# Optimization experiments

Hardware: AMD Instinct MI355X
Metric: run time of the kernel (lower is better)

## Reference

```python
import jax, jax.numpy as jnp
import numpy as np

D_MODEL = 1024
N_HEAD = 16
D_K = D_MODEL // N_HEAD
D_FF = 2048
EPS = 1e-6
SCALE = np.sqrt(D_K).astype(np.float32)


def layer_norm(x, alpha, beta):
    # Faithful to source: unbiased std (ddof=1), eps added to std
    mean = jnp.mean(x, axis=-1, keepdims=True)
    std = jnp.std(x, axis=-1, keepdims=True, ddof=1) + EPS
    return alpha * (x - mean) / std + beta


def setup_inputs() -> dict:
    key = jax.random.key(0)
    ks = jax.random.split(key, 12)
    s = 0.02
    return {
        "x": jax.random.normal(ks[0], (4, 1024, D_MODEL), dtype=jnp.float32),
        "Wq": jax.random.normal(ks[1], (D_MODEL, D_MODEL), dtype=jnp.float32) * s,
        "bq": jax.random.normal(ks[2], (D_MODEL,), dtype=jnp.float32) * s,
        "Wo": jax.random.normal(ks[3], (D_MODEL, D_MODEL), dtype=jnp.float32) * s,
        "bo": jax.random.normal(ks[4], (D_MODEL,), dtype=jnp.float32) * s,
        "W1": jax.random.normal(ks[5], (D_MODEL, D_FF), dtype=jnp.float32) * s,
        "b1": jax.random.normal(ks[6], (D_FF,), dtype=jnp.float32) * s,
        "W2": jax.random.normal(ks[7], (D_FF, D_MODEL), dtype=jnp.float32) * s,
        "b2": jax.random.normal(ks[8], (D_MODEL,), dtype=jnp.float32) * s,
        "alpha": jnp.ones((D_MODEL,), dtype=jnp.float32),
        "beta": jnp.ones((D_MODEL,), dtype=jnp.float32),
    }


def reference(x, Wq, bq, Wo, bo, W1, b1, W2, b2, alpha, beta):
    b, s, d = x.shape
    # Source bug kept: q, k, v all use q_linear
    def proj(t):
        return (t @ Wq + bq).reshape(b, s, N_HEAD, D_K).transpose(0, 2, 1, 3)
    q = proj(x)  # [b,h,s,dk]
    k = proj(x)
    v = proj(x)
    scores = jnp.einsum('bhqd,bhkd->bhqk', q, k) / SCALE
    scores = jax.nn.softmax(scores, axis=-1)
    z = jnp.einsum('bhqk,bhkd->bhqd', scores, v)
    concat = z.transpose(0, 2, 1, 3).reshape(b, s, d)
    attn_out = concat @ Wo + bo
    x = layer_norm(x + attn_out, alpha, beta)
    ff = jax.nn.relu(x @ W1 + b1) @ W2 + b2
    x = layer_norm(x + ff, alpha, beta)  # source reuses norm_1
    return x
```

## Files before the change

### kernel.cpp

```cpp
#include <hip/hip_runtime.h>
#include <hip/hip_bf16.h>
#include <stdint.h>

#define TOK   4096
#define DMODEL 1024
#define DFF    2048
#define NHEAD  16
#define DK     64

typedef unsigned short u16;
typedef __attribute__((ext_vector_type(8))) short short8;
typedef __attribute__((ext_vector_type(4))) float f32x4;

typedef __attribute__((address_space(1))) void gvoid;
typedef __attribute__((address_space(3))) void lvoid;

#define QSCALE   0.35355339f
#define QUNSCALE 2.82842712f

__device__ __forceinline__ u16 f2b(float f) {
    uint32_t x = __builtin_bit_cast(uint32_t, f);
    x += 0x7FFFu + ((x >> 16) & 1u);
    return (u16)(x >> 16);
}
__device__ __forceinline__ float b2f(u16 u) {
    uint32_t x = ((uint32_t)u) << 16;
    return __builtin_bit_cast(float, x);
}
__device__ __forceinline__ uint32_t f2b2(float lo, float hi) {
    return (uint32_t)f2b(lo) | ((uint32_t)f2b(hi) << 16);
}

__device__ __forceinline__ void gload16(const void* g, void* l) {
    __builtin_amdgcn_global_load_lds((gvoid*)g, (lvoid*)l, 16, 0, 0);
}

__device__ __forceinline__ void cvt_tr_dev(
    const float* __restrict__ W, u16* __restrict__ Wt, int K, int N,
    int bx, int by, int tid, u16 T[64][68])
{
    const int tx = tid & 15, ty = tid >> 4;
    const int n0 = bx * 64, k0 = by * 64;
#pragma unroll
    for (int i = 0; i < 4; i++) {
        int k = ty + i * 16;
        float4 v = *(const float4*)&W[(size_t)(k0 + k) * N + n0 + tx * 4];
        T[tx * 4 + 0][k] = f2b(v.x);
        T[tx * 4 + 1][k] = f2b(v.y);
        T[tx * 4 + 2][k] = f2b(v.z);
        T[tx * 4 + 3][k] = f2b(v.w);
    }
    __syncthreads();
#pragma unroll
    for (int i = 0; i < 4; i++) {
        int n = ty + i * 16;
        ushort4 o;
        o.x = T[n][tx * 4 + 0]; o.y = T[n][tx * 4 + 1];
        o.z = T[n][tx * 4 + 2]; o.w = T[n][tx * 4 + 3];
        *(ushort4*)&Wt[(size_t)(n0 + n) * K + k0 + tx * 4] = o;
    }
}

__global__ __launch_bounds__(256) void prep_all(
    const float* __restrict__ Wq, const float* __restrict__ Wo,
    const float* __restrict__ W1, const float* __restrict__ W2,
    u16* __restrict__ Wqt, u16* __restrict__ Wot,
    u16* __restrict__ W1t, u16* __restrict__ W2t,
    const float* __restrict__ x, u16* __restrict__ xb)
{
    __shared__ u16 T[64][68];
    const int id = blockIdx.x, tid = threadIdx.x;
    if (id < 256) {
        cvt_tr_dev(Wq, Wqt, 1024, 1024, id & 15, id >> 4, tid, T);
    } else if (id < 512) {
        int t = id - 256;
        cvt_tr_dev(Wo, Wot, 1024, 1024, t & 15, t >> 4, tid, T);
    } else if (id < 1024) {
        int t = id - 512;
        cvt_tr_dev(W1, W1t, 1024, 2048, t & 31, t >> 5, tid, T);
    } else if (id < 1536) {
        int t = id - 1024;
        cvt_tr_dev(W2, W2t, 2048, 1024, t & 15, t >> 4, tid, T);
    } else {
        size_t base = (size_t)(id - 1536) * 1024 + tid;
#pragma unroll
        for (int j = 0; j < 4; j++) {
            float4 v = ((const float4*)x)[base + j * 256];
            ((uint2*)xb)[base + j * 256] =
                make_uint2(f2b2(v.x, v.y), f2b2(v.z, v.w));
        }
    }
}

template<int BM, int BN, bool RELU, bool OUTBF16, bool QOUT>
__global__ __launch_bounds__(256) void gemm_mfma(
    const u16* __restrict__ A, const u16* __restrict__ Bt,
    const float* __restrict__ bias, void* __restrict__ Cv,
    u16* __restrict__ CT, float oscale,
    int M, int N, int K)
{
    constexpr int MF = BM / 32;
    constexpr int NF = BN / 32;
    constexpr int ASTR = BM * 64;
    constexpr int BSTR = BN * 64;
    __shared__ __align__(16) u16 As[2 * ASTR];
    __shared__ __align__(16) u16 Bs[2 * BSTR];

    const int tid  = threadIdx.x;
    const int lane = tid & 63;
    const int wid  = tid >> 6;
    const int wm = wid >> 1, wn = wid & 1;
    const int frow = lane & 15, fk = lane >> 4;

    const int gx = N / BN;
    const int gy = M / BM;
    const int rpx = gy >> 3;
    const int L = blockIdx.x;
    const int xcd = L & 7, within = L >> 3;
    const int yy = xcd * rpx + within / gx;
    const int xx = within % gx;

    const int row0 = yy * BM;
    const int col0 = xx * BN;

    const u16* gA[MF]; u16* lA[MF];
    const u16* gB[NF]; u16* lB[NF];
#pragma unroll
    for (int inst = 0; inst < MF; inst++) {
        int s = inst * 256 + tid;
        int r = s >> 3;
        int kc = ((s & 7) ^ (r & 7)) * 8;
        gA[inst] = A + (size_t)(row0 + r) * K + kc;
        lA[inst] = As + inst * 2048 + wid * 512;
    }
#pragma unroll
    for (int inst = 0; inst < NF; inst++) {
        int s = inst * 256 + tid;
        int r = s >> 3;
        int kc = ((s & 7) ^ (r & 7)) * 8;
        gB[inst] = Bt + (size_t)(col0 + r) * K + kc;
        lB[inst] = Bs + inst * 2048 + wid * 512;
    }

    int aoff[MF][2], boff[NF][2];
#pragma unroll
    for (int m = 0; m < MF; m++) {
        int r = wm * (BM / 2) + m * 16 + frow;
#pragma unroll
        for (int kk = 0; kk < 2; kk++)
            aoff[m][kk] = r * 64 + (((kk << 2) + fk) ^ (r & 7)) * 8;
    }
#pragma unroll
    for (int n = 0; n < NF; n++) {
        int r = wn * (BN / 2) + n * 16 + frow;
#pragma unroll
        for (int kk = 0; kk < 2; kk++)
            boff[n][kk] = r * 64 + (((kk << 2) + fk) ^ (r & 7)) * 8;
    }

    f32x4 acc[MF][NF] = {};
    const int nT = K >> 6;

#pragma unroll
    for (int inst = 0; inst < MF; inst++) gload16(gA[inst], lA[inst]);
#pragma unroll
    for (int inst = 0; inst < NF; inst++) gload16(gB[inst], lB[inst]);
    __syncthreads();

    for (int t = 0; t < nT; t++) {
        const int cur = t & 1;
        if (t + 1 < nT) {
            const int k0 = (t + 1) << 6;
#pragma unroll
            for (int inst = 0; inst < MF; inst++)
                gload16(gA[inst] + k0, lA[inst] + (cur ^ 1) * ASTR);
#pragma unroll
            for (int inst = 0; inst < NF; inst++)
                gload16(gB[inst] + k0, lB[inst] + (cur ^ 1) * BSTR);
        }

        const u16* Ab = As + cur * ASTR;
        const u16* Bb = Bs + cur * BSTR;
        short8 a[MF][2], b[NF][2];
#pragma unroll
        for (int m = 0; m < MF; m++)
#pragma unroll
            for (int kk = 0; kk < 2; kk++)
                a[m][kk] = *(const short8*)(Ab + aoff[m][kk]);
#pragma unroll
        for (int n = 0; n < NF; n++)
#pragma unroll
            for (int kk = 0; kk < 2; kk++)
                b[n][kk] = *(const short8*)(Bb + boff[n][kk]);

#pragma unroll
        for (int m = 0; m < MF; m++)
#pragma unroll
            for (int n = 0; n < NF; n++)
#pragma unroll
                for (int kk = 0; kk < 2; kk++)
                    acc[m][n] = __builtin_amdgcn_mfma_f32_16x16x32_bf16(
                        a[m][kk], b[n][kk], acc[m][n], 0, 0, 0);

        __syncthreads();
    }

#pragma unroll
    for (int n = 0; n < NF; n++) {
        const int gcol = col0 + wn * (BN / 2) + n * 16 + frow;
        const float bv = bias[gcol];
#pragma unroll
        for (int m = 0; m < MF; m++) {
            const int grow0 = row0 + wm * (BM / 2) + m * 16 + fk * 4;
            float v[4];
#pragma unroll
            for (int i = 0; i < 4; i++) {
                v[i] = (acc[m][n][i] + bv) * oscale;
                if (RELU) v[i] = fmaxf(v[i], 0.0f);
                if (OUTBF16)
                    ((u16*)Cv)[(size_t)(grow0 + i) * N + gcol] = f2b(v[i]);
                else
                    ((float*)Cv)[(size_t)(grow0 + i) * N + gcol] = v[i];
            }
            if (QOUT) {
                const int hh = gcol >> 6, d = gcol & 63;
                const int bb = grow0 >> 10, sl = grow0 & 1023;
                *(uint2*)&CT[(((size_t)(bb * 16 + hh) * 64 + d) << 10) + sl] =
                    make_uint2(f2b2(v[0], v[1]), f2b2(v[2], v[3]));
            }
        }
    }
}

__global__ __launch_bounds__(256, 2) void attn_mfma(
    const u16* __restrict__ qb, const u16* __restrict__ qT,
    u16* __restrict__ zb)
{
    __shared__ __align__(16) u16 Ks[2][64 * 64];
    __shared__ __align__(16) u16 Kt[2][64 * 64];
    __shared__ __align__(16) u16 Ps[128 * 64];

    const int tid  = threadIdx.x;
    const int lane = tid & 63;
    const int w    = tid >> 6;
    const int frow = lane & 15, fk = lane >> 4;

    const int h  = blockIdx.x;
    const int qt = blockIdx.y;
    const int b  = blockIdx.z;
    const int q0 = qt * 128;

    const u16* qhead = qb + ((size_t)b * 1024) * 1024 + h * 64;
    const u16* thead = qT + ((size_t)(b * 16 + h) * 64) * 1024;

#pragma unroll
    for (int inst = 0; inst < 2; inst++) {
        int s = inst * 256 + tid, r = s >> 3, kc = ((s & 7) ^ (r & 7)) * 8;
        gload16(qhead + (size_t)r * 1024 + kc, Ks[0] + inst * 2048 + w * 512);
        gload16(thead + (size_t)r * 1024 + kc, Kt[0] + inst * 2048 + w * 512);
    }

    short8 qf[2][2];
#pragma unroll
    for (int m = 0; m < 2; m++) {
        int r = q0 + w * 32 + m * 16 + frow;
#pragma unroll
        for (int kk = 0; kk < 2; kk++)
            qf[m][kk] = *(const short8*)(qhead + (size_t)r * 1024 + kk * 32 + fk * 8);
    }

    float lp[2] = {};
    f32x4 o[2][4] = {};

    __syncthreads();

    for (int t = 0; t < 16; t++) {
        const int cur = t & 1;
        if (t < 15) {
            const int kv = (t + 1) * 64;
#pragma unroll
            for (int inst = 0; inst < 2; inst++) {
                int s = inst * 256 + tid, r = s >> 3, kc = ((s & 7) ^ (r & 7)) * 8;
                gload16(qhead + (size_t)(kv + r) * 1024 + kc,
                        Ks[cur ^ 1] + inst * 2048 + w * 512);
                gload16(thead + (size_t)r * 1024 + kv + kc,
                        Kt[cur ^ 1] + inst * 2048 + w * 512);
            }
        }

        short8 kf[4][2];
#pragma unroll
        for (int n = 0; n < 4; n++) {
            int r = n * 16 + frow;
#pragma unroll
            for (int kk = 0; kk < 2; kk++)
                kf[n][kk] = *(const short8*)(Ks[cur] + r * 64 +
                                             (((kk << 2) + fk) ^ (r & 7)) * 8);
        }
        f32x4 st[4][2] = {};
#pragma unroll
        for (int nk = 0; nk < 4; nk++)
#pragma unroll
            for (int mq = 0; mq < 2; mq++)
#pragma unroll
                for (int kk = 0; kk < 2; kk++)
                    st[nk][mq] = __builtin_amdgcn_mfma_f32_16x16x32_bf16(
                        kf[nk][kk], qf[mq][kk], st[nk][mq], 0, 0, 0);

#pragma unroll
        for (int mq = 0; mq < 2; mq++) {
            const int r = w * 32 + mq * 16 + frow;
            const int rb = r * 64, sw = (r & 7) << 3;
#pragma unroll
            for (int nk = 0; nk < 4; nk++) {
                float p0 = __expf(st[nk][mq][0]);
                float p1 = __expf(st[nk][mq][1]);
                float p2 = __expf(st[nk][mq][2]);
                float p3 = __expf(st[nk][mq][3]);
                lp[mq] += (p0 + p1) + (p2 + p3);
                *(uint2*)&Ps[rb + ((nk * 16 + fk * 4) ^ sw)] =
                    make_uint2(f2b2(p0, p1), f2b2(p2, p3));
            }
        }

        short8 pa[2][2], vf[4][2];
#pragma unroll
        for (int m = 0; m < 2; m++) {
            int r = w * 32 + m * 16 + frow;
#pragma unroll
            for (int kk = 0; kk < 2; kk++)
                pa[m][kk] = *(const short8*)(Ps + r * 64 +
                                             (((kk << 2) + fk) ^ (r & 7)) * 8);
        }
#pragma unroll
        for (int n = 0; n < 4; n++) {
            int r = n * 16 + frow;
#pragma unroll
            for (int kk = 0; kk < 2; kk++)
                vf[n][kk] = *(const short8*)(Kt[cur] + r * 64 +
                                             (((kk << 2) + fk) ^ (r & 7)) * 8);
        }
#pragma unroll
        for (int m = 0; m < 2; m++)
#pragma unroll
            for (int n = 0; n < 4; n++)
#pragma unroll
                for (int kk = 0; kk < 2; kk++)
                    o[m][n] = __builtin_amdgcn_mfma_f32_16x16x32_bf16(
                        pa[m][kk], vf[n][kk], o[m][n], 0, 0, 0);

        __syncthreads();
    }

#pragma unroll
    for (int mq = 0; mq < 2; mq++) {
        lp[mq] += __shfl_xor(lp[mq], 16);
        lp[mq] += __shfl_xor(lp[mq], 32);
    }
#pragma unroll
    for (int m = 0; m < 2; m++)
#pragma unroll
        for (int i = 0; i < 4; i++) {
            const float lfull = __shfl(lp[m], fk * 4 + i);
            const float rl = QUNSCALE / lfull;
            const size_t gr = (size_t)(b * 1024 + q0 + w * 32 + m * 16 + fk * 4 + i);
#pragma unroll
            for (int n = 0; n < 4; n++)
                zb[gr * 1024 + h * 64 + n * 16 + frow] = f2b(o[m][n][i] * rl);
        }
}

__device__ __forceinline__ float4 ld4(const float* p) { return *(const float4*)p; }
__device__ __forceinline__ float4 ld4(const u16* p) {
    ushort4 u = *(const ushort4*)p;
    return make_float4(b2f(u.x), b2f(u.y), b2f(u.z), b2f(u.w));
}
__device__ __forceinline__ void st4(float* p, float4 v) { *(float4*)p = v; }
__device__ __forceinline__ void st4(u16* p, float4 v) {
    *(uint2*)p = make_uint2(f2b2(v.x, v.y), f2b2(v.z, v.w));
}

template<typename TA, typename TB, typename TO>
__global__ __launch_bounds__(256) void add_ln(
    const TA* __restrict__ a, const TB* __restrict__ b,
    const float* __restrict__ alpha, const float* __restrict__ beta,
    TO* __restrict__ out)
{
    const int row = blockIdx.x;
    const int c = threadIdx.x * 4;
    float4 va = ld4(a + (size_t)row * DMODEL + c);
    float4 vb = ld4(b + (size_t)row * DMODEL + c);
    float v0 = va.x + vb.x, v1 = va.y + vb.y;
    float v2 = va.z + vb.z, v3 = va.w + vb.w;

    float sum = (v0 + v1) + (v2 + v3);
    float sq  = (v0 * v0 + v1 * v1) + (v2 * v2 + v3 * v3);
#pragma unroll
    for (int off = 32; off > 0; off >>= 1) {
        sum += __shfl_xor(sum, off);
        sq  += __shfl_xor(sq, off);
    }
    __shared__ float s1[4], s2[4];
    const int wid = threadIdx.x >> 6, lane = threadIdx.x & 63;
    if (lane == 0) { s1[wid] = sum; s2[wid] = sq; }
    __syncthreads();
    sum = (s1[0] + s1[1]) + (s1[2] + s1[3]);
    sq  = (s2[0] + s2[1]) + (s2[2] + s2[3]);

    const float mean = sum * (1.0f / 1024.0f);
    float var = (sq - 1024.0f * mean * mean) * (1.0f / 1023.0f);
    var = fmaxf(var, 0.0f);
    const float rdenom = 1.0f / (sqrtf(var) + 1e-6f);

    float4 al = *(const float4*)(alpha + c);
    float4 be = *(const float4*)(beta + c);
    float4 r;
    r.x = al.x * (v0 - mean) * rdenom + be.x;
    r.y = al.y * (v1 - mean) * rdenom + be.y;
    r.z = al.z * (v2 - mean) * rdenom + be.z;
    r.w = al.w * (v3 - mean) * rdenom + be.w;
    st4(out + (size_t)row * DMODEL + c, r);
}

extern "C" void kernel_launch(void* const* d_in, const int* in_sizes, int n_in,
                              void* d_out, int out_size, void* d_ws, size_t ws_size,
                              hipStream_t stream) {
    const float* x     = (const float*)d_in[0];
    const float* Wq    = (const float*)d_in[1];
    const float* bq    = (const float*)d_in[2];
    const float* Wo    = (const float*)d_in[3];
    const float* bo    = (const float*)d_in[4];
    const float* W1    = (const float*)d_in[5];
    const float* b1    = (const float*)d_in[6];
    const float* W2    = (const float*)d_in[7];
    const float* b2    = (const float*)d_in[8];
    const float* alpha = (const float*)d_in[9];
    const float* beta  = (const float*)d_in[10];

    char* base = (char*)d_ws;
    u16* Wqt = (u16*)base;
    u16* Wot = (u16*)(base + (2u  << 20));
    u16* W1t = (u16*)(base + (4u  << 20));
    u16* W2t = (u16*)(base + (8u  << 20));
    u16* zb  = (u16*)(base + (12u << 20));
    u16* x1b = zb;
    u16* qb  = (u16*)(base + (20u << 20));
    u16* g2  = qb;
    u16* qT  = (u16*)(base + (28u << 20));
    u16* xb  = (u16*)(base + (36u << 20));
    u16* g   = xb;
    u16* hb  = (u16*)(base + (36u << 20));

    dim3 blk(256);

    prep_all<<<dim3(2560), blk, 0, stream>>>(
        Wq, Wo, W1, W2, Wqt, Wot, W1t, W2t, x, xb);

    gemm_mfma<64, 64, false, true, true><<<dim3(1024), blk, 0, stream>>>(
        xb, Wqt, bq, qb, qT, QSCALE, TOK, 1024, 1024);
    attn_mfma<<<dim3(16, 8, 4), blk, 0, stream>>>(qb, qT, zb);
    gemm_mfma<64, 64, false, true, false><<<dim3(1024), blk, 0, stream>>>(
        zb, Wot, bo, g, nullptr, 1.0f, TOK, 1024, 1024);
    add_ln<float, u16, u16><<<dim3(TOK), blk, 0, stream>>>(x, g, alpha, beta, x1b);
    gemm_mfma<64, 128, true, true, false><<<dim3(1024), blk, 0, stream>>>(
        x1b, W1t, b1, hb, nullptr, 1.0f, TOK, 2048, 1024);
    gemm_mfma<64, 64, false, true, false><<<dim3(1024), blk, 0, stream>>>(
        hb, W2t, b2, g2, nullptr, 1.0f, TOK, 1024, 2048);
    add_ln<u16, u16, float><<<dim3(TOK), blk, 0, stream>>>(
        x1b, g2, alpha, beta, (float*)d_out);
}
```

Baseline: 147.4 us.

## Load K/V fragments directly from global in attention, dropping LDS staging

```diff
diff --git a/kernel.cpp b/kernel.cpp
--- a/kernel.cpp
+++ b/kernel.cpp
@@ -232,12 +232,10 @@
     }
 }
 
-__global__ __launch_bounds__(256, 2) void attn_mfma(
+__global__ __launch_bounds__(256, 3) void attn_mfma(
     const u16* __restrict__ qb, const u16* __restrict__ qT,
     u16* __restrict__ zb)
 {
-    __shared__ __align__(16) u16 Ks[2][64 * 64];
-    __shared__ __align__(16) u16 Kt[2][64 * 64];
     __shared__ __align__(16) u16 Ps[128 * 64];
 
     const int tid  = threadIdx.x;
@@ -253,13 +251,6 @@
     const u16* qhead = qb + ((size_t)b * 1024) * 1024 + h * 64;
     const u16* thead = qT + ((size_t)(b * 16 + h) * 64) * 1024;
 
-#pragma unroll
-    for (int inst = 0; inst < 2; inst++) {
-        int s = inst * 256 + tid, r = s >> 3, kc = ((s & 7) ^ (r & 7)) * 8;
-        gload16(qhead + (size_t)r * 1024 + kc, Ks[0] + inst * 2048 + w * 512);
-        gload16(thead + (size_t)r * 1024 + kc, Kt[0] + inst * 2048 + w * 512);
-    }
-
     short8 qf[2][2];
 #pragma unroll
     for (int m = 0; m < 2; m++) {
@@ -272,31 +263,25 @@
     float lp[2] = {};
     f32x4 o[2][4] = {};
 
-    __syncthreads();
-
     for (int t = 0; t < 16; t++) {
-        const int cur = t & 1;
-        if (t < 15) {
-            const int kv = (t + 1) * 64;
-#pragma unroll
-            for (int inst = 0; inst < 2; inst++) {
-                int s = inst * 256 + tid, r = s >> 3, kc = ((s & 7) ^ (r & 7)) * 8;
-                gload16(qhead + (size_t)(kv + r) * 1024 + kc,
-                        Ks[cur ^ 1] + inst * 2048 + w * 512);
-                gload16(thead + (size_t)r * 1024 + kv + kc,
-                        Kt[cur ^ 1] + inst * 2048 + w * 512);
-            }
-        }
+        const int kv0 = t * 64;
+
+        short8 vf[4][2];
+#pragma unroll
+        for (int n = 0; n < 4; n++)
+#pragma unroll
+            for (int kk = 0; kk < 2; kk++)
+                vf[n][kk] = *(const short8*)(thead +
+                    (size_t)(n * 16 + frow) * 1024 + kv0 + kk * 32 + fk * 8);
 
         short8 kf[4][2];
 #pragma unroll
-        for (int n = 0; n < 4; n++) {
-            int r = n * 16 + frow;
+        for (int n = 0; n < 4; n++)
 #pragma unroll
             for (int kk = 0; kk < 2; kk++)
-                kf[n][kk] = *(const short8*)(Ks[cur] + r * 64 +
-                                             (((kk << 2) + fk) ^ (r & 7)) * 8);
-        }
+                kf[n][kk] = *(const short8*)(qhead +
+                    (size_t)(kv0 + n * 16 + frow) * 1024 + kk * 32 + fk * 8);
+
         f32x4 st[4][2] = {};
 #pragma unroll
         for (int nk = 0; nk < 4; nk++)
@@ -323,7 +308,7 @@
             }
         }
 
-        short8 pa[2][2], vf[4][2];
+        short8 pa[2][2];
 #pragma unroll
         for (int m = 0; m < 2; m++) {
             int r = w * 32 + m * 16 + frow;
@@ -333,14 +318,6 @@
                                              (((kk << 2) + fk) ^ (r & 7)) * 8);
         }
 #pragma unroll
-        for (int n = 0; n < 4; n++) {
-            int r = n * 16 + frow;
-#pragma unroll
-            for (int kk = 0; kk < 2; kk++)
-                vf[n][kk] = *(const short8*)(Kt[cur] + r * 64 +
-                                             (((kk << 2) + fk) ^ (r & 7)) * 8);
-        }
-#pragma unroll
         for (int m = 0; m < 2; m++)
 #pragma unroll
             for (int n = 0; n < 4; n++)
@@ -348,8 +325,6 @@
                 for (int kk = 0; kk < 2; kk++)
                     o[m][n] = __builtin_amdgcn_mfma_f32_16x16x32_bf16(
                         pa[m][kk], vf[n][kk], o[m][n], 0, 0, 0);
-
-        __syncthreads();
     }
 
 #pragma unroll
```

Result: slower. 178.0 us (+20.8%).
